# Kernel tuning notes

Measured on AMD Instinct MI355X. Metric: run time of the kernel, lower is better.

## Reference

```python
import jax, jax.numpy as jnp
import numpy as np

B, N, L, H, N_NODE, STEP = 512, 50, 50, 128, 100000, 1


def setup_inputs() -> dict:
    key = jax.random.key(0)
    ks = jax.random.split(key, 24)
    stdv = 1.0 / np.sqrt(H)
    u = lambda k, shape: jax.random.uniform(k, shape, jnp.float32, -stdv, stdv)
    inp = {
        "items": jax.random.randint(ks[0], (B, N), 0, N_NODE),
        "A": jax.random.uniform(ks[1], (B, N, 2 * N), jnp.float32),
        "alias_inputs": jax.random.randint(ks[2], (B, L), 0, N),
        "embedding": u(ks[3], (N_NODE, H)),
        "w_ih": u(ks[4], (3 * H, 2 * H)),
        "w_hh": u(ks[5], (3 * H, H)),
        "b_ih": u(ks[6], (3 * H,)),
        "b_hh": u(ks[7], (3 * H,)),
        "b_iah": u(ks[8], (H,)),
        "b_oah": u(ks[9], (H,)),
        "W_ein": u(ks[10], (H, H)), "b_ein": u(ks[11], (H,)),
        "W_eout": u(ks[12], (H, H)), "b_eout": u(ks[13], (H,)),
        "W1": u(ks[14], (H, H)), "b1": u(ks[15], (H,)),
        "W2": u(ks[16], (H, H)), "b2": u(ks[17], (H,)),
        "W3": u(ks[18], (1, H)),
        "Wt": u(ks[19], (H, 2 * H)), "bt": u(ks[20], (H,)),
    }
    return inp


def reference(items, A, alias_inputs, embedding, w_ih, w_hh, b_ih, b_hh,
              b_iah, b_oah, W_ein, b_ein, W_eout, b_eout,
              W1, b1, W2, b2, W3, Wt, bt):
    hidden = embedding[items]  # [B,N,H]
    A_in, A_out = A[:, :, :N], A[:, :, N:2 * N]
    for _ in range(STEP):
        # GRU-style GNN cell
        h_in = jnp.matmul(A_in, hidden @ W_ein.T + b_ein) + b_iah   # [B,N,H]
        h_out = jnp.matmul(A_out, hidden @ W_eout.T + b_eout) + b_oah
        inputs = jnp.concatenate([h_in, h_out], axis=2)             # [B,N,2H]
        gi = inputs @ w_ih.T + b_ih                                  # [B,N,3H]
        gh = hidden @ w_hh.T + b_hh
        i_r, i_i, i_n = jnp.split(gi, 3, axis=2)
        h_r, h_i, h_n = jnp.split(gh, 3, axis=2)
        resetgate = jax.nn.sigmoid(i_r + h_r)
        inputgate = jax.nn.sigmoid(i_i + h_i)
        newgate = jnp.tanh(i_n + resetgate * h_n)
        hidden = newgate + inputgate * (hidden - newgate)
    # gather per-position node states: seq_hidden[b, l] = hidden[b, alias[b, l]]
    mask = alias_inputs > 0  # [B,L]
    idx = jnp.broadcast_to(alias_inputs[:, :, None], (B, L, H))
    seq_hidden = jnp.take_along_axis(hidden, idx, axis=1)  # [B,L,H]
    last = jnp.sum(mask, axis=1) - 1
    ht = seq_hidden[jnp.arange(B), last]  # [B,H]
    # attention pooling
    q1 = (ht @ W1.T + b1)[:, None, :]      # [B,1,H]
    q2 = seq_hidden @ W2.T + b2            # [B,L,H]
    alpha = jax.nn.sigmoid(q1 + q2) @ W3.T  # [B,L,1]
    a = jnp.sum(alpha * seq_hidden * mask[:, :, None].astype(seq_hidden.dtype), axis=1)
    a = jnp.concatenate([a, ht], axis=1) @ Wt.T + bt  # [B,H]
    scores = a @ embedding[1:].T  # [B, n_node-1]
    return scores
```

## Files before the change

kernel.cpp:

```cpp
#include <hip/hip_runtime.h>

#define NB   512
#define NN   50
#define LLn  50
#define HD   128
#define OUTN 99999

#define WS_W1T   0
#define WS_W2T   65536
#define WS_WTT   131072
#define WS_WEH   262144
#define WS_WEL   327680
#define WS_WCATH 393216
#define WS_WCATL 688128
#define WS_AHI   983040
#define WS_ALO   1114112

typedef __attribute__((ext_vector_type(8))) short bf16x8;
typedef __attribute__((ext_vector_type(4))) float f32x4;

__device__ __forceinline__ unsigned short f2bf(float f) {
  unsigned int u = __float_as_uint(f);
  unsigned int r = (u + 0x7FFFu + ((u >> 16) & 1u)) >> 16;
  return (unsigned short)r;
}
__device__ __forceinline__ float bf2f(unsigned short h) {
  return __uint_as_float(((unsigned int)h) << 16);
}
__device__ __forceinline__ void cvt4(float4 v, ushort4& hi, ushort4& lo) {
  unsigned short h0 = f2bf(v.x), h1 = f2bf(v.y), h2 = f2bf(v.z), h3 = f2bf(v.w);
  hi = make_ushort4(h0, h1, h2, h3);
  lo = make_ushort4(f2bf(v.x - bf2f(h0)), f2bf(v.y - bf2f(h1)),
                    f2bf(v.z - bf2f(h2)), f2bf(v.w - bf2f(h3)));
}
__device__ __forceinline__ void gl_lds16(const void* g, void* l) {
  __builtin_amdgcn_global_load_lds(
      (const __attribute__((address_space(1))) void*)g,
      (__attribute__((address_space(3))) void*)l, 16, 0, 0);
}
__device__ __forceinline__ float sigm(float x) { return 1.f/(1.f + __expf(-x)); }

__global__ void k0_prep(const float* __restrict__ w_ih, const float* __restrict__ w_hh,
                        const float* __restrict__ W_ein, const float* __restrict__ W_eout,
                        const float* __restrict__ W1, const float* __restrict__ W2,
                        const float* __restrict__ Wt, char* __restrict__ wsb)
{
  float* wsf = (float*)wsb;
  for (int i = blockIdx.x * blockDim.x + threadIdx.x; i < 245760; i += gridDim.x * blockDim.x) {
    int idx = i;
    if (idx < 16384) { int k = idx >> 7, c = idx & 127; wsf[idx] = W1[c*128 + k]; continue; }
    idx -= 16384;
    if (idx < 16384) { int k = idx >> 7, c = idx & 127; wsf[16384 + idx] = W2[c*128 + k]; continue; }
    idx -= 16384;
    if (idx < 32768) { int k = idx >> 7, c = idx & 127; wsf[32768 + idx] = Wt[c*256 + k]; continue; }
    idx -= 32768;
    if (idx < 32768) {
      int n = idx >> 7, k = idx & 127;
      float v = (n < 128) ? W_ein[n*128 + k] : W_eout[(n-128)*128 + k];
      unsigned short h = f2bf(v);
      *(unsigned short*)(wsb + WS_WEH + idx*2) = h;
      *(unsigned short*)(wsb + WS_WEL + idx*2) = f2bf(v - bf2f(h));
      continue;
    }
    idx -= 32768;
    {
      int n = idx / 384, k = idx % 384;
      float v = (k < 256) ? w_ih[n*256 + k] : w_hh[n*128 + (k - 256)];
      unsigned short h = f2bf(v);
      *(unsigned short*)(wsb + WS_WCATH + idx*2) = h;
      *(unsigned short*)(wsb + WS_WCATL + idx*2) = f2bf(v - bf2f(h));
    }
  }
}

__global__ __launch_bounds__(512) void k1f(const int* __restrict__ items,
    const float* __restrict__ A, const float* __restrict__ emb,
    const int* __restrict__ alias_in,
    const float* __restrict__ b_ein, const float* __restrict__ b_eout,
    const float* __restrict__ b_iah, const float* __restrict__ b_oah,
    const float* __restrict__ b_ih, const float* __restrict__ b_hh,
    const float* __restrict__ b1, const float* __restrict__ b2,
    const float* __restrict__ W3, const float* __restrict__ bt_,
    char* __restrict__ wsb)
{
  extern __shared__ char lds[];
  char*  HH   = lds;
  char*  HL   = lds + 16384;
  float* ALDS = (float*)(lds + 32768);
  float* HEf  = (float*)(lds + 53568);
  float* INf  = (float*)(lds + 104768);
  char*  STGH = lds + 53568;
  char*  STGL = lds + 53568 + 16384;
  float* H2f  = (float*)(lds + 104768);
  float* SIG  = (float*)(lds + 53568);
  float* Q1P  = (float*)(lds + 86336);
  float* AP   = (float*)(lds + 88384);
  float* RP   = (float*)(lds + 90432);
  float* ALP  = (float*)(lds + 92480);
  int*   ALI  = (int*)(lds + 92736);

  const int b = blockIdx.x, tid = threadIdx.x;
  const int lane = tid & 63, wid = tid >> 6, l15 = lane & 15, lq = lane >> 4;

  {
    const float* Ab = A + (size_t)b*NN*100;
    for (int i = tid; i < 5000; i += 512) {
      int n = i / 100, cc = i % 100;
      int s_ = (cc >= 50) ? 1 : 0, m = cc - s_*50;
      ALDS[s_*2600 + n*52 + m] = Ab[i];
    }
    for (int i = tid; i < 1600; i += 512) {
      int row = i >> 5, part = i & 31;
      int it = items[b*NN + row];
      float4 v = *(const float4*)&emb[(size_t)it*128 + part*4];
      ushort4 h4, g4;
      cvt4(v, h4, g4);
      unsigned off = row*256 + (((unsigned)(part*8)) ^ (((unsigned)(row&7)) << 4));
      *(ushort4*)(HH + off) = h4;
      *(ushort4*)(HL + off) = g4;
    }
    for (int i = tid; i < 224; i += 512) {
      int row = 50 + (i >> 4), part = i & 15;
      unsigned off = row*256 + (((unsigned)(part*16)) ^ (((unsigned)(row&7)) << 4));
      *(ushort4*)(HH + off) = make_ushort4(0,0,0,0);
      *(ushort4*)(HL + off) = make_ushort4(0,0,0,0);
    }
  }
  __syncthreads();

  {
    f32x4 acc2[4][2];
#pragma unroll
    for (int i = 0; i < 4; ++i) { acc2[i][0] = (f32x4){0,0,0,0}; acc2[i][1] = (f32x4){0,0,0,0}; }
    for (int s = 0; s < 4; ++s) {
      bf16x8 ah[4], al[4];
#pragma unroll
      for (int i = 0; i < 4; ++i) {
        int row = i*16 + l15;
        unsigned off = row*256 + (((unsigned)(s*64 + lq*16)) ^ (((unsigned)(row&7)) << 4));
        ah[i] = *(const bf16x8*)(HH + off);
        al[i] = *(const bf16x8*)(HL + off);
      }
#pragma unroll
      for (int j = 0; j < 2; ++j) {
        int n = wid*32 + j*16 + l15;
        unsigned boff = (unsigned)(n*256 + s*64 + lq*16);
        bf16x8 bh = *(const bf16x8*)(wsb + WS_WEH + boff);
        bf16x8 bl = *(const bf16x8*)(wsb + WS_WEL + boff);
#pragma unroll
        for (int i = 0; i < 4; ++i) {
          acc2[i][j] = __builtin_amdgcn_mfma_f32_16x16x32_bf16(ah[i], bh, acc2[i][j], 0,0,0);
          acc2[i][j] = __builtin_amdgcn_mfma_f32_16x16x32_bf16(ah[i], bl, acc2[i][j], 0,0,0);
          acc2[i][j] = __builtin_amdgcn_mfma_f32_16x16x32_bf16(al[i], bh, acc2[i][j], 0,0,0);
        }
      }
    }
#pragma unroll
    for (int j = 0; j < 2; ++j) {
      int n = wid*32 + j*16 + l15;
      float bias = (n < 128) ? b_ein[n] : b_eout[n - 128];
#pragma unroll
      for (int i = 0; i < 4; ++i) {
        int rb = i*16 + lq*4;
#pragma unroll
        for (int q = 0; q < 4; ++q) {
          int row = rb + q;
          if (row < 50) HEf[row*256 + n] = acc2[i][j][q] + bias;
        }
      }
    }
  }
  __syncthreads();

  {
    const int c = tid & 127, sel = (tid >> 7) & 1, th = tid >> 8;
    const float* Asel = ALDS + sel*2600;
    const float* hes  = HEf + sel*128 + c;
    const int nbase = th*25;
    float acc[25];
#pragma unroll
    for (int n = 0; n < 25; ++n) acc[n] = 0.f;
    for (int m4 = 0; m4 < 48; m4 += 4) {
      float x0 = hes[(m4+0)*256], x1 = hes[(m4+1)*256];
      float x2 = hes[(m4+2)*256], x3 = hes[(m4+3)*256];
#pragma unroll
      for (int n = 0; n < 25; ++n) {
        float4 a = *(const float4*)&Asel[(nbase+n)*52 + m4];
        acc[n] += a.x*x0 + a.y*x1 + a.z*x2 + a.w*x3;
      }
    }
    {
      float x0 = hes[48*256], x1 = hes[49*256];
#pragma unroll
      for (int n = 0; n < 25; ++n)
        acc[n] += Asel[(nbase+n)*52 + 48]*x0 + Asel[(nbase+n)*52 + 49]*x1;
    }
    float bias = sel ? b_oah[c] : b_iah[c];
#pragma unroll
    for (int n = 0; n < 25; ++n)
      INf[(nbase+n)*256 + sel*128 + c] = acc[n] + bias;
  }
  __syncthreads();

  f32x4 accRI[4][2], accNi[4], accNh[4];
#pragma unroll
  for (int i = 0; i < 4; ++i) {
    accRI[i][0] = (f32x4){0,0,0,0}; accRI[i][1] = (f32x4){0,0,0,0};
    accNi[i] = (f32x4){0,0,0,0};    accNh[i] = (f32x4){0,0,0,0};
  }

  for (int kh = 0; kh < 3; ++kh) {
    const char* AH;
    const char* AL;
    if (kh < 2) {
      if (kh == 1) __syncthreads();
      for (int i2 = tid; i2 < 2048; i2 += 512) {
        int row = i2 >> 5, part = i2 & 31;
        float4 v = (row < 50) ? *(const float4*)&INf[row*256 + kh*128 + part*4]
                              : make_float4(0.f,0.f,0.f,0.f);
        ushort4 h4, g4;
        cvt4(v, h4, g4);
        unsigned off = row*256 + (((unsigned)(part*8)) ^ (((unsigned)(row&7)) << 4));
        *(ushort4*)(STGH + off) = h4;
        *(ushort4*)(STGL + off) = g4;
      }
      __syncthreads();
      AH = STGH; AL = STGL;
    } else {
      AH = HH; AL = HL;
    }

    for (int s = 0; s < 4; ++s) {
      bf16x8 ah[4], al[4];
#pragma unroll
      for (int i = 0; i < 4; ++i) {
        int row = i*16 + l15;
        unsigned off = row*256 + (((unsigned)(s*64 + lq*16)) ^ (((unsigned)(row&7)) << 4));
        ah[i] = *(const bf16x8*)(AH + off);
        al[i] = *(const bf16x8*)(AL + off);
      }
      const int ng = wid*16 + l15;
#pragma unroll
      for (int g = 0; g < 2; ++g) {
        int n = g*128 + ng;
        unsigned boff = (unsigned)(n*768 + kh*256 + s*64 + lq*16);
        bf16x8 bh = *(const bf16x8*)(wsb + WS_WCATH + boff);
        bf16x8 bl = *(const bf16x8*)(wsb + WS_WCATL + boff);
#pragma unroll
        for (int i = 0; i < 4; ++i) {
          accRI[i][g] = __builtin_amdgcn_mfma_f32_16x16x32_bf16(ah[i], bh, accRI[i][g], 0,0,0);
          accRI[i][g] = __builtin_amdgcn_mfma_f32_16x16x32_bf16(ah[i], bl, accRI[i][g], 0,0,0);
          accRI[i][g] = __builtin_amdgcn_mfma_f32_16x16x32_bf16(al[i], bh, accRI[i][g], 0,0,0);
        }
      }
      {
        int n = 256 + ng;
        unsigned boff = (unsigned)(n*768 + kh*256 + s*64 + lq*16);
        bf16x8 bh = *(const bf16x8*)(wsb + WS_WCATH + boff);
        bf16x8 bl = *(const bf16x8*)(wsb + WS_WCATL + boff);
        if (kh < 2) {
#pragma unroll
          for (int i = 0; i < 4; ++i) {
            accNi[i] = __builtin_amdgcn_mfma_f32_16x16x32_bf16(ah[i], bh, accNi[i], 0,0,0);
            accNi[i] = __builtin_amdgcn_mfma_f32_16x16x32_bf16(ah[i], bl, accNi[i], 0,0,0);
            accNi[i] = __builtin_amdgcn_mfma_f32_16x16x32_bf16(al[i], bh, accNi[i], 0,0,0);
          }
        } else {
#pragma unroll
          for (int i = 0; i < 4; ++i) {
            accNh[i] = __builtin_amdgcn_mfma_f32_16x16x32_bf16(ah[i], bh, accNh[i], 0,0,0);
            accNh[i] = __builtin_amdgcn_mfma_f32_16x16x32_bf16(ah[i], bl, accNh[i], 0,0,0);
            accNh[i] = __builtin_amdgcn_mfma_f32_16x16x32_bf16(al[i], bh, accNh[i], 0,0,0);
          }
        }
      }
    }
  }

  {
    const int c = wid*16 + l15;
    float bir = b_ih[c], bii = b_ih[128+c], bin_ = b_ih[256+c];
    float bhr = b_hh[c], bhi = b_hh[128+c], bhn  = b_hh[256+c];
#pragma unroll
    for (int i = 0; i < 4; ++i) {
#pragma unroll
      for (int q = 0; q < 4; ++q) {
        int row = i*16 + lq*4 + q;
        if (row < 50) {
          float rg = sigm(accRI[i][0][q] + bir + bhr);
          float ig = sigm(accRI[i][1][q] + bii + bhi);
          float ng_ = tanhf(accNi[i][q] + bin_ + rg*(accNh[i][q] + bhn));
          unsigned byte = row*256 + (((unsigned)(c*2)) ^ (((unsigned)(row&7)) << 4));
          float h = bf2f(*(const unsigned short*)(HH + byte))
                  + bf2f(*(const unsigned short*)(HL + byte));
          H2f[row*132 + c] = ng_ + ig*(h - ng_);
        }
      }
    }
  }
  if (tid < LLn) ALI[tid] = alias_in[b*LLn + tid];
  __syncthreads();

  int cnt = 0;
  for (int l = 0; l < LLn; ++l) cnt += (ALI[l] > 0) ? 1 : 0;
  int last = cnt - 1; if (last < 0) last = LLn - 1;
  const int a_last = ALI[last];

  const int c = tid & 127, h4 = tid >> 7;
  const float* W1T = (const float*)(wsb + WS_W1T);
  const float* W2T = (const float*)(wsb + WS_W2T);
  const float* WtT = (const float*)(wsb + WS_WTT);

  {
    float q = 0.f;
    for (int k = h4*32; k < h4*32 + 32; k += 4) {
      float4 x = *(const float4*)&H2f[a_last*132 + k];
      q += x.x*W1T[(k<<7)+c] + x.y*W1T[((k+1)<<7)+c]
         + x.z*W1T[((k+2)<<7)+c] + x.w*W1T[((k+3)<<7)+c];
    }
    Q1P[h4*128 + c] = q;
  }
  __syncthreads();

  {
    int al_[13];
#pragma unroll
    for (int ii = 0; ii < 13; ++ii) {
      int l = h4 + 4*ii;
      al_[ii] = (l < LLn) ? ALI[l] : 0;
    }
    float q2a[13];
#pragma unroll
    for (int ii = 0; ii < 13; ++ii) q2a[ii] = 0.f;
    for (int k = 0; k < HD; k += 4) {
      float w0 = W2T[(k<<7)+c],     w1 = W2T[((k+1)<<7)+c];
      float w2 = W2T[((k+2)<<7)+c], w3 = W2T[((k+3)<<7)+c];
#pragma unroll
      for (int ii = 0; ii < 13; ++ii) {
        float4 x = *(const float4*)&H2f[al_[ii]*132 + k];
        q2a[ii] += x.x*w0; q2a[ii] += x.y*w1; q2a[ii] += x.z*w2; q2a[ii] += x.w*w3;
      }
    }
    float q1c = Q1P[c] + Q1P[128+c] + Q1P[256+c] + Q1P[384+c] + b1[c] + b2[c];
#pragma unroll
    for (int ii = 0; ii < 13; ++ii) {
      int l = h4 + 4*ii;
      if (l < LLn) SIG[l*132 + c] = sigm(q1c + q2a[ii]);
    }
  }
  __syncthreads();

  if (tid < 400) {
    int l = tid >> 3, qd = tid & 7;
    float sum = 0.f;
    for (int cc = qd*16; cc < qd*16 + 16; cc += 4) {
      float4 x = *(const float4*)&SIG[l*132 + cc];
      sum += x.x*W3[cc] + x.y*W3[cc+1] + x.z*W3[cc+2] + x.w*W3[cc+3];
    }
    sum += __shfl_xor(sum, 1);
    sum += __shfl_xor(sum, 2);
    sum += __shfl_xor(sum, 4);
    if (qd == 0) ALP[l] = (ALI[l] > 0) ? sum : 0.f;
  }
  __syncthreads();

  {
    float acc = 0.f;
    int l0 = h4*13, l1 = l0 + 13; if (l1 > LLn) l1 = LLn;
    for (int l = l0; l < l1; ++l)
      acc += ALP[l] * H2f[ALI[l]*132 + c];
    AP[h4*128 + c] = acc;
  }
  __syncthreads();

  {
    float r = 0.f;
    for (int k = h4*32; k < h4*32 + 32; ++k) {
      float av = AP[k] + AP[128+k] + AP[256+k] + AP[384+k];
      r += av * WtT[(k<<7) + c] + H2f[a_last*132 + k] * WtT[((128+k)<<7) + c];
    }
    RP[h4*128 + c] = r;
  }
  __syncthreads();

  if (tid < 128) {
    float r = bt_[c] + RP[c] + RP[128+c] + RP[256+c] + RP[384+c];
    int kh = c >> 6, kl = c & 63;
    unsigned int cb = (unsigned int)(kl*2) ^ (((unsigned int)(b & 7)) << 4);
    unsigned short hi = f2bf(r);
    unsigned short lo = f2bf(r - bf2f(hi));
    *(unsigned short*)(wsb + WS_AHI + kh*65536 + b*128 + cb) = hi;
    *(unsigned short*)(wsb + WS_ALO + kh*65536 + b*128 + cb) = lo;
  }
}

__global__ __launch_bounds__(512) void k2_mfma(const float* __restrict__ emb,
                                               const char* __restrict__ wsb,
                                               float* __restrict__ out)
{
  extern __shared__ char ldsc[];
  char* AHI = ldsc;
  char* ALO = ldsc + 32768;
  char* EHI = ldsc + 65536;
  char* ELO = ldsc + 81920;

  const int tid  = threadIdx.x;
  const int lane = tid & 63;
  const int wid  = tid >> 6;
  const int wm   = wid >> 1;
  const int wn   = wid & 1;
  const int j0   = blockIdx.x * 128;
  const int l15  = lane & 15, lq = lane >> 4;

  f32x4 acc[2][4][4];
#pragma unroll
  for (int bi = 0; bi < 2; ++bi)
#pragma unroll
    for (int i = 0; i < 4; ++i)
#pragma unroll
      for (int j = 0; j < 4; ++j) acc[bi][i][j] = (f32x4){0.f, 0.f, 0.f, 0.f};

  for (int kh = 0; kh < 2; ++kh) {
    {
      int rbase = tid >> 4, c4 = tid & 15;
#pragma unroll
      for (int rr = 0; rr < 4; ++rr) {
        int row = rbase + rr*32;
        int j = j0 + row; if (j > OUTN - 1) j = OUTN - 1;
        float4 v = *(const float4*)&emb[(size_t)(1 + j)*HD + kh*64 + c4*4];
        ushort4 hi4, lo4;
        cvt4(v, hi4, lo4);
        unsigned int off = (unsigned int)(row*128) + (((unsigned int)(c4*8)) ^ (((unsigned int)(row&7)) << 4));
        *(ushort4*)(EHI + off) = hi4;
        *(ushort4*)(ELO + off) = lo4;
      }
    }
#pragma unroll
    for (int bi = 0; bi < 2; ++bi) {
      const char* srcH = wsb + WS_AHI + kh*65536 + bi*32768;
      const char* srcL = wsb + WS_ALO + kh*65536 + bi*32768;
#pragma unroll
      for (int r = 0; r < 4; ++r) {
        int off = (r*512 + tid) * 16;
        gl_lds16(srcH + off, AHI + off);
        gl_lds16(srcL + off, ALO + off);
      }
      __syncthreads();

#pragma unroll
      for (int s = 0; s < 2; ++s) {
        bf16x8 ah[4], al[4], bh[4], bl[4];
        const unsigned int cb = (unsigned int)(s*64 + (lq << 4));
#pragma unroll
        for (int i = 0; i < 4; ++i) {
          int row = wm*64 + i*16 + l15;
          unsigned int off = (unsigned int)(row*128) + (cb ^ (((unsigned int)(row&7)) << 4));
          ah[i] = *(const bf16x8*)(AHI + off);
          al[i] = *(const bf16x8*)(ALO + off);
        }
#pragma unroll
        for (int j = 0; j < 4; ++j) {
          int row = wn*64 + j*16 + l15;
          unsigned int off = (unsigned int)(row*128) + (cb ^ (((unsigned int)(row&7)) << 4));
          bh[j] = *(const bf16x8*)(EHI + off);
          bl[j] = *(const bf16x8*)(ELO + off);
        }
#pragma unroll
        for (int i = 0; i < 4; ++i)
#pragma unroll
          for (int j = 0; j < 4; ++j) {
            acc[bi][i][j] = __builtin_amdgcn_mfma_f32_16x16x32_bf16(ah[i], bh[j], acc[bi][i][j], 0, 0, 0);
            acc[bi][i][j] = __builtin_amdgcn_mfma_f32_16x16x32_bf16(ah[i], bl[j], acc[bi][i][j], 0, 0, 0);
            acc[bi][i][j] = __builtin_amdgcn_mfma_f32_16x16x32_bf16(al[i], bh[j], acc[bi][i][j], 0, 0, 0);
          }
      }
      __syncthreads();
    }
  }

#pragma unroll
  for (int bi = 0; bi < 2; ++bi)
#pragma unroll
    for (int i = 0; i < 4; ++i) {
#pragma unroll
      for (int j = 0; j < 4; ++j) {
        int jj = j0 + wn*64 + j*16 + l15;
        if (jj < OUTN) {
          size_t rowbase = (size_t)(bi*256 + wm*64 + i*16 + lq*4);
#pragma unroll
          for (int q = 0; q < 4; ++q)
            out[(rowbase + q)*OUTN + jj] = acc[bi][i][j][q];
        }
      }
    }
}

extern "C" void kernel_launch(void* const* d_in, const int* in_sizes, int n_in,
                              void* d_out, int out_size, void* d_ws, size_t ws_size,
                              hipStream_t stream)
{
  const int*   items  = (const int*)  d_in[0];
  const float* A      = (const float*)d_in[1];
  const int*   alias  = (const int*)  d_in[2];
  const float* emb    = (const float*)d_in[3];
  const float* w_ih   = (const float*)d_in[4];
  const float* w_hh   = (const float*)d_in[5];
  const float* b_ih   = (const float*)d_in[6];
  const float* b_hh   = (const float*)d_in[7];
  const float* b_iah  = (const float*)d_in[8];
  const float* b_oah  = (const float*)d_in[9];
  const float* W_ein  = (const float*)d_in[10];
  const float* b_ein  = (const float*)d_in[11];
  const float* W_eout = (const float*)d_in[12];
  const float* b_eout = (const float*)d_in[13];
  const float* W1     = (const float*)d_in[14];
  const float* b1     = (const float*)d_in[15];
  const float* W2     = (const float*)d_in[16];
  const float* b2     = (const float*)d_in[17];
  const float* W3     = (const float*)d_in[18];
  const float* Wt     = (const float*)d_in[19];
  const float* bt_    = (const float*)d_in[20];

  char*  wsb  = (char*)d_ws;
  float* outf = (float*)d_out;

  k0_prep<<<240, 256, 0, stream>>>(w_ih, w_hh, W_ein, W_eout, W1, W2, Wt, wsb);

  k1f<<<NB, 512, 155968, stream>>>(items, A, emb, alias, b_ein, b_eout, b_iah, b_oah,
                                   b_ih, b_hh, b1, b2, W3, bt_, wsb);

  k2_mfma<<<dim3(782, 1), 512, 98304, stream>>>(emb, (const char*)d_ws, outf);
}
```

Before: 206.9 us.

## Restructure GNN kernel into per-direction phases to halve LDS footprint

The fused per-session kernel now handles the in and out edge directions one after the other. Each direction runs its hidden GEMM, then the adjacency multiply, then the GRU input GEMM. The adjacency matrix is read straight from global memory instead of being staged in LDS, and the adjacency product is written directly as split bf16 hi/lo images, which removes the separate conversion pass. LDS use drops from about 156KB to 77KB so two blocks can share a CU, at the cost of extra barriers, non-coalesced global reads of A, and more serialised phases.

```diff
diff --git a/kernel.cpp b/kernel.cpp
--- a/kernel.cpp
+++ b/kernel.cpp
@@ -15,6 +15,7 @@
 #define WS_WCATL 688128
 #define WS_AHI   983040
 #define WS_ALO   1114112
+
 
 typedef __attribute__((ext_vector_type(8))) short bf16x8;
 typedef __attribute__((ext_vector_type(4))) float f32x4;
@@ -85,53 +86,38 @@
 {
   extern __shared__ char lds[];
   char*  HH   = lds;
-  char*  HL   = lds + 16384;
-  float* ALDS = (float*)(lds + 32768);
-  float* HEf  = (float*)(lds + 53568);
-  float* INf  = (float*)(lds + 104768);
-  char*  STGH = lds + 53568;
-  char*  STGL = lds + 53568 + 16384;
-  float* H2f  = (float*)(lds + 104768);
-  float* SIG  = (float*)(lds + 53568);
-  float* Q1P  = (float*)(lds + 86336);
-  float* AP   = (float*)(lds + 88384);
-  float* RP   = (float*)(lds + 90432);
-  float* ALP  = (float*)(lds + 92480);
-  int*   ALI  = (int*)(lds + 92736);
+  char*  HL   = lds + 12800;
+  char*  IMGH = lds + 25600;
+  char*  IMGL = lds + 38400;
+  float* HEf  = (float*)(lds + 51200);
+  float* H2f  = (float*)(lds + 25600);
+  float* SIG  = (float*)(lds + 51200);
+  float* Q1P  = (float*)(lds + 0);
+  float* AP   = (float*)(lds + 2048);
+  float* RP   = (float*)(lds + 4096);
+  float* ALP  = (float*)(lds + 6144);
+  int*   ALI  = (int*)(lds + 6400);
 
   const int b = blockIdx.x, tid = threadIdx.x;
   const int lane = tid & 63, wid = tid >> 6, l15 = lane & 15, lq = lane >> 4;
 
-  {
-    const float* Ab = A + (size_t)b*NN*100;
-    for (int i = tid; i < 5000; i += 512) {
-      int n = i / 100, cc = i % 100;
-      int s_ = (cc >= 50) ? 1 : 0, m = cc - s_*50;
-      ALDS[s_*2600 + n*52 + m] = Ab[i];
-    }
-    for (int i = tid; i < 1600; i += 512) {
-      int row = i >> 5, part = i & 31;
-      int it = items[b*NN + row];
-      float4 v = *(const float4*)&emb[(size_t)it*128 + part*4];
-      ushort4 h4, g4;
-      cvt4(v, h4, g4);
-      unsigned off = row*256 + (((unsigned)(part*8)) ^ (((unsigned)(row&7)) << 4));
-      *(ushort4*)(HH + off) = h4;
-      *(ushort4*)(HL + off) = g4;
-    }
-    for (int i = tid; i < 224; i += 512) {
-      int row = 50 + (i >> 4), part = i & 15;
-      unsigned off = row*256 + (((unsigned)(part*16)) ^ (((unsigned)(row&7)) << 4));
-      *(ushort4*)(HH + off) = make_ushort4(0,0,0,0);
-      *(ushort4*)(HL + off) = make_ushort4(0,0,0,0);
-    }
-  }
-  __syncthreads();
-
-  {
-    f32x4 acc2[4][2];
-#pragma unroll
-    for (int i = 0; i < 4; ++i) { acc2[i][0] = (f32x4){0,0,0,0}; acc2[i][1] = (f32x4){0,0,0,0}; }
+  for (int i = tid; i < 1600; i += 512) {
+    int row = i >> 5, part = i & 31;
+    int it = items[b*NN + row];
+    float4 v = *(const float4*)&emb[(size_t)it*128 + part*4];
+    ushort4 h4v, g4v;
+    cvt4(v, h4v, g4v);
+    unsigned off = row*256 + (((unsigned)(part*8)) ^ (((unsigned)(row&7)) << 4));
+    *(ushort4*)(HH + off) = h4v;
+    *(ushort4*)(HL + off) = g4v;
+  }
+  __syncthreads();
+
+  auto he_gemm = [&](int nb, const float* __restrict__ bias) {
+    f32x4 a2[4];
+#pragma unroll
+    for (int i = 0; i < 4; ++i) a2[i] = (f32x4){0.f,0.f,0.f,0.f};
+    const int n = wid*16 + l15;
     for (int s = 0; s < 4; ++s) {
       bf16x8 ah[4], al[4];
 #pragma unroll
@@ -141,66 +127,74 @@
         ah[i] = *(const bf16x8*)(HH + off);
         al[i] = *(const bf16x8*)(HL + off);
       }
-#pragma unroll
-      for (int j = 0; j < 2; ++j) {
-        int n = wid*32 + j*16 + l15;
-        unsigned boff = (unsigned)(n*256 + s*64 + lq*16);
-        bf16x8 bh = *(const bf16x8*)(wsb + WS_WEH + boff);
-        bf16x8 bl = *(const bf16x8*)(wsb + WS_WEL + boff);
-#pragma unroll
-        for (int i = 0; i < 4; ++i) {
-          acc2[i][j] = __builtin_amdgcn_mfma_f32_16x16x32_bf16(ah[i], bh, acc2[i][j], 0,0,0);
-          acc2[i][j] = __builtin_amdgcn_mfma_f32_16x16x32_bf16(ah[i], bl, acc2[i][j], 0,0,0);
-          acc2[i][j] = __builtin_amdgcn_mfma_f32_16x16x32_bf16(al[i], bh, acc2[i][j], 0,0,0);
-        }
-      }
-    }
-#pragma unroll
-    for (int j = 0; j < 2; ++j) {
-      int n = wid*32 + j*16 + l15;
-      float bias = (n < 128) ? b_ein[n] : b_eout[n - 128];
+      unsigned boff = (unsigned)((nb + n)*256 + s*64 + lq*16);
+      bf16x8 bh = *(const bf16x8*)(wsb + WS_WEH + boff);
+      bf16x8 bl = *(const bf16x8*)(wsb + WS_WEL + boff);
 #pragma unroll
       for (int i = 0; i < 4; ++i) {
-        int rb = i*16 + lq*4;
-#pragma unroll
-        for (int q = 0; q < 4; ++q) {
-          int row = rb + q;
-          if (row < 50) HEf[row*256 + n] = acc2[i][j][q] + bias;
-        }
-      }
-    }
-  }
-  __syncthreads();
-
-  {
-    const int c = tid & 127, sel = (tid >> 7) & 1, th = tid >> 8;
-    const float* Asel = ALDS + sel*2600;
-    const float* hes  = HEf + sel*128 + c;
-    const int nbase = th*25;
-    float acc[25];
-#pragma unroll
-    for (int n = 0; n < 25; ++n) acc[n] = 0.f;
+        a2[i] = __builtin_amdgcn_mfma_f32_16x16x32_bf16(ah[i], bh, a2[i], 0,0,0);
+        a2[i] = __builtin_amdgcn_mfma_f32_16x16x32_bf16(ah[i], bl, a2[i], 0,0,0);
+        a2[i] = __builtin_amdgcn_mfma_f32_16x16x32_bf16(al[i], bh, a2[i], 0,0,0);
+      }
+    }
+    float bv = bias[n];
+#pragma unroll
+    for (int i = 0; i < 4; ++i)
+#pragma unroll
+      for (int q = 0; q < 4; ++q) {
+        int row = i*16 + lq*4 + q;
+        if (row < 50) HEf[row*128 + (n ^ ((row&3)<<2))] = a2[i][q] + bv;
+      }
+  };
+
+  auto a_mul = [&](int sel, const float* __restrict__ biasv) {
+    const int c = tid & 127, th = tid >> 7;
+    const int nbase = th*13;
+    const int cnt = (th == 3) ? 11 : 13;
+    const float* Ab = A + (size_t)b*NN*100 + sel*50;
+    float acc[13];
+#pragma unroll
+    for (int n = 0; n < 13; ++n) acc[n] = 0.f;
     for (int m4 = 0; m4 < 48; m4 += 4) {
-      float x0 = hes[(m4+0)*256], x1 = hes[(m4+1)*256];
-      float x2 = hes[(m4+2)*256], x3 = hes[(m4+3)*256];
-#pragma unroll
-      for (int n = 0; n < 25; ++n) {
-        float4 a = *(const float4*)&Asel[(nbase+n)*52 + m4];
-        acc[n] += a.x*x0 + a.y*x1 + a.z*x2 + a.w*x3;
+      float x0 = HEf[(m4+0)*128 + (c ^ (((m4+0)&3)<<2))];
+      float x1 = HEf[(m4+1)*128 + (c ^ (((m4+1)&3)<<2))];
+      float x2 = HEf[(m4+2)*128 + (c ^ (((m4+2)&3)<<2))];
+      float x3 = HEf[(m4+3)*128 + (c ^ (((m4+3)&3)<<2))];
+#pragma unroll
+      for (int n = 0; n < 13; ++n) {
+        if (n < cnt) {
+          const float* ar = Ab + (nbase+n)*100 + m4;
+          float2 a01 = *(const float2*)ar;
+          float2 a23 = *(const float2*)(ar + 2);
+          acc[n] += a01.x*x0 + a01.y*x1 + a23.x*x2 + a23.y*x3;
+        }
       }
     }
     {
-      float x0 = hes[48*256], x1 = hes[49*256];
-#pragma unroll
-      for (int n = 0; n < 25; ++n)
-        acc[n] += Asel[(nbase+n)*52 + 48]*x0 + Asel[(nbase+n)*52 + 49]*x1;
-    }
-    float bias = sel ? b_oah[c] : b_iah[c];
-#pragma unroll
-    for (int n = 0; n < 25; ++n)
-      INf[(nbase+n)*256 + sel*128 + c] = acc[n] + bias;
-  }
-  __syncthreads();
+      float x0 = HEf[48*128 + c];
+      float x1 = HEf[49*128 + (c ^ 4)];
+#pragma unroll
+      for (int n = 0; n < 13; ++n) {
+        if (n < cnt) {
+          float2 a01 = *(const float2*)(Ab + (nbase+n)*100 + 48);
+          acc[n] += a01.x*x0 + a01.y*x1;
+        }
+      }
+    }
+    float bv = biasv[c];
+#pragma unroll
+    for (int n = 0; n < 13; ++n) {
+      if (n < cnt) {
+        float v = acc[n] + bv;
+        int row = nbase + n;
+        unsigned short hi = f2bf(v);
+        unsigned short lo = f2bf(v - bf2f(hi));
+        unsigned byte = row*256 + (((unsigned)(c*2)) ^ (((unsigned)(row&7)) << 4));
+        *(unsigned short*)(IMGH + byte) = hi;
+        *(unsigned short*)(IMGL + byte) = lo;
+      }
+    }
+  };
 
   f32x4 accRI[4][2], accNi[4], accNh[4];
 #pragma unroll
@@ -209,27 +203,8 @@
     accNi[i] = (f32x4){0,0,0,0};    accNh[i] = (f32x4){0,0,0,0};
   }
 
-  for (int kh = 0; kh < 3; ++kh) {
-    const char* AH;
-    const char* AL;
-    if (kh < 2) {
-      if (kh == 1) __syncthreads();
-      for (int i2 = tid; i2 < 2048; i2 += 512) {
-        int row = i2 >> 5, part = i2 & 31;
-        float4 v = (row < 50) ? *(const float4*)&INf[row*256 + kh*128 + part*4]
-                              : make_float4(0.f,0.f,0.f,0.f);
-        ushort4 h4, g4;
-        cvt4(v, h4, g4);
-        unsigned off = row*256 + (((unsigned)(part*8)) ^ (((unsigned)(row&7)) << 4));
-        *(ushort4*)(STGH + off) = h4;
-        *(ushort4*)(STGL + off) = g4;
-      }
-      __syncthreads();
-      AH = STGH; AL = STGL;
-    } else {
-      AH = HH; AL = HL;
-    }
-
+  auto cat_gemm = [&](const char* AH, const char* AL, int kh, bool toNh) {
+    const int nl = wid*16 + l15;
     for (int s = 0; s < 4; ++s) {
       bf16x8 ah[4], al[4];
 #pragma unroll
@@ -239,11 +214,9 @@
         ah[i] = *(const bf16x8*)(AH + off);
         al[i] = *(const bf16x8*)(AL + off);
       }
-      const int ng = wid*16 + l15;
 #pragma unroll
       for (int g = 0; g < 2; ++g) {
-        int n = g*128 + ng;
-        unsigned boff = (unsigned)(n*768 + kh*256 + s*64 + lq*16);
+        unsigned boff = (unsigned)((g*128 + nl)*768 + kh*256 + s*64 + lq*16);
         bf16x8 bh = *(const bf16x8*)(wsb + WS_WCATH + boff);
         bf16x8 bl = *(const bf16x8*)(wsb + WS_WCATL + boff);
 #pragma unroll
@@ -254,28 +227,35 @@
         }
       }
       {
-        int n = 256 + ng;
-        unsigned boff = (unsigned)(n*768 + kh*256 + s*64 + lq*16);
+        unsigned boff = (unsigned)((256 + nl)*768 + kh*256 + s*64 + lq*16);
         bf16x8 bh = *(const bf16x8*)(wsb + WS_WCATH + boff);
         bf16x8 bl = *(const bf16x8*)(wsb + WS_WCATL + boff);
-        if (kh < 2) {
+        if (toNh) {
+#pragma unroll
+          for (int i = 0; i < 4; ++i) {
+            accNh[i] = __builtin_amdgcn_mfma_f32_16x16x32_bf16(ah[i], bh, accNh[i], 0,0,0);
+            accNh[i] = __builtin_amdgcn_mfma_f32_16x16x32_bf16(ah[i], bl, accNh[i], 0,0,0);
+            accNh[i] = __builtin_amdgcn_mfma_f32_16x16x32_bf16(al[i], bh, accNh[i], 0,0,0);
+          }
+        } else {
 #pragma unroll
           for (int i = 0; i < 4; ++i) {
             accNi[i] = __builtin_amdgcn_mfma_f32_16x16x32_bf16(ah[i], bh, accNi[i], 0,0,0);
             accNi[i] = __builtin_amdgcn_mfma_f32_16x16x32_bf16(ah[i], bl, accNi[i], 0,0,0);
             accNi[i] = __builtin_amdgcn_mfma_f32_16x16x32_bf16(al[i], bh, accNi[i], 0,0,0);
           }
-        } else {
-#pragma unroll
-          for (int i = 0; i < 4; ++i) {
-            accNh[i] = __builtin_amdgcn_mfma_f32_16x16x32_bf16(ah[i], bh, accNh[i], 0,0,0);
-            accNh[i] = __builtin_amdgcn_mfma_f32_16x16x32_bf16(ah[i], bl, accNh[i], 0,0,0);
-            accNh[i] = __builtin_amdgcn_mfma_f32_16x16x32_bf16(al[i], bh, accNh[i], 0,0,0);
-          }
-        }
-      }
-    }
-  }
+        }
+      }
+    }
+  };
+
+  he_gemm(0, b_ein);            __syncthreads();
+  a_mul(0, b_iah);              __syncthreads();
+  cat_gemm(IMGH, IMGL, 0, false); __syncthreads();
+  he_gemm(128, b_eout);         __syncthreads();
+  a_mul(1, b_oah);              __syncthreads();
+  cat_gemm(IMGH, IMGL, 1, false);
+  cat_gemm(HH, HL, 2, true);    __syncthreads();
 
   {
     const int c = wid*16 + l15;
@@ -293,11 +273,13 @@
           unsigned byte = row*256 + (((unsigned)(c*2)) ^ (((unsigned)(row&7)) << 4));
           float h = bf2f(*(const unsigned short*)(HH + byte))
                   + bf2f(*(const unsigned short*)(HL + byte));
-          H2f[row*132 + c] = ng_ + ig*(h - ng_);
-        }
-      }
-    }
-  }
+          H2f[row*128 + c] = ng_ + ig*(h - ng_);
+        }
+      }
+    }
+  }
+  __syncthreads();
+
   if (tid < LLn) ALI[tid] = alias_in[b*LLn + tid];
   __syncthreads();
 
@@ -314,7 +296,7 @@
   {
     float q = 0.f;
     for (int k = h4*32; k < h4*32 + 32; k += 4) {
-      float4 x = *(const float4*)&H2f[a_last*132 + k];
+      float4 x = *(const float4*)&H2f[a_last*128 + k];
       q += x.x*W1T[(k<<7)+c] + x.y*W1T[((k+1)<<7)+c]
          + x.z*W1T[((k+2)<<7)+c] + x.w*W1T[((k+3)<<7)+c];
     }
@@ -337,15 +319,15 @@
       float w2 = W2T[((k+2)<<7)+c], w3 = W2T[((k+3)<<7)+c];
 #pragma unroll
       for (int ii = 0; ii < 13; ++ii) {
-        float4 x = *(const float4*)&H2f[al_[ii]*132 + k];
-        q2a[ii] += x.x*w0; q2a[ii] += x.y*w1; q2a[ii] += x.z*w2; q2a[ii] += x.w*w3;
+        float4 x = *(const float4*)&H2f[al_[ii]*128 + k];
+        q2a[ii] += x.x*w0 + x.y*w1 + x.z*w2 + x.w*w3;
       }
     }
     float q1c = Q1P[c] + Q1P[128+c] + Q1P[256+c] + Q1P[384+c] + b1[c] + b2[c];
 #pragma unroll
     for (int ii = 0; ii < 13; ++ii) {
       int l = h4 + 4*ii;
-      if (l < LLn) SIG[l*132 + c] = sigm(q1c + q2a[ii]);
+      if (l < LLn) SIG[l*128 + c] = sigm(q1c + q2a[ii]);
     }
   }
   __syncthreads();
@@ -354,7 +336,7 @@
     int l = tid >> 3, qd = tid & 7;
     float sum = 0.f;
     for (int cc = qd*16; cc < qd*16 + 16; cc += 4) {
-      float4 x = *(const float4*)&SIG[l*132 + cc];
+      float4 x = *(const float4*)&SIG[l*128 + cc];
       sum += x.x*W3[cc] + x.y*W3[cc+1] + x.z*W3[cc+2] + x.w*W3[cc+3];
     }
     sum += __shfl_xor(sum, 1);
@@ -368,7 +350,7 @@
     float acc = 0.f;
     int l0 = h4*13, l1 = l0 + 13; if (l1 > LLn) l1 = LLn;
     for (int l = l0; l < l1; ++l)
-      acc += ALP[l] * H2f[ALI[l]*132 + c];
+      acc += ALP[l] * H2f[ALI[l]*128 + c];
     AP[h4*128 + c] = acc;
   }
   __syncthreads();
@@ -377,7 +359,7 @@
     float r = 0.f;
     for (int k = h4*32; k < h4*32 + 32; ++k) {
       float av = AP[k] + AP[128+k] + AP[256+k] + AP[384+k];
-      r += av * WtT[(k<<7) + c] + H2f[a_last*132 + k] * WtT[((128+k)<<7) + c];
+      r += av * WtT[(k<<7) + c] + H2f[a_last*128 + k] * WtT[((128+k)<<7) + c];
     }
     RP[h4*128 + c] = r;
   }
@@ -526,8 +508,8 @@
 
   k0_prep<<<240, 256, 0, stream>>>(w_ih, w_hh, W_ein, W_eout, W1, W2, Wt, wsb);
 
-  k1f<<<NB, 512, 155968, stream>>>(items, A, emb, alias, b_ein, b_eout, b_iah, b_oah,
-                                   b_ih, b_hh, b1, b2, W3, bt_, wsb);
+  k1f<<<NB, 512, 76800, stream>>>(items, A, emb, alias, b_ein, b_eout, b_iah, b_oah,
+                                  b_ih, b_hh, b1, b2, W3, bt_, wsb);
 
   k2_mfma<<<dim3(782, 1), 512, 98304, stream>>>(emb, (const char*)d_ws, outf);
 }
```

Result: slower. 722.1 us (+249.0%).
